# Kernel optimization log

Hardware: AMD Instinct MI355X
Metric: run time of the kernel (lower is better)

## Reference

```python
import jax, jax.numpy as jnp
import numpy as np

B, T, C, H = 2, 2048, 1024, 16

def setup_inputs() -> dict:
    key = jax.random.key(0)
    ks = jax.random.split(key, 6)
    s = 1.0 / np.sqrt(C)
    return {
        "x": jax.random.normal(ks[0], (B, T, C), jnp.float32),
        "Wq": jax.random.normal(ks[1], (C, C), jnp.float32) * s,
        "Wk": jax.random.normal(ks[2], (C, C), jnp.float32) * s,
        "Wv": jax.random.normal(ks[3], (C, C), jnp.float32) * s,
        "Wp": jax.random.normal(ks[4], (C, C), jnp.float32) * s,
        "bp": jnp.zeros((C,), jnp.float32),
    }

def reference(x, Wq, Wk, Wv, Wp, bp):
    b, t, c = x.shape
    hd = c // H  # head dim
    # Linear layers: torch nn.Linear computes x @ W.T
    def split_heads(y):
        return y.reshape(b, t, H, hd).transpose(0, 2, 1, 3)  # [B,H,T,hd]
    q = split_heads(x @ Wq.T)
    k = split_heads(x @ Wk.T)
    v = split_heads(x @ Wv.T)
    scale = hd ** -0.5
    wei = jnp.einsum('bhqd,bhkd->bhqk', q, k) * scale  # [B,H,T,T]
    causal = jnp.tril(jnp.ones((t, t), bool))
    wei = jnp.where(causal, wei, -jnp.inf)
    wei = jax.nn.softmax(wei, axis=-1)
    out = jnp.einsum('bhqk,bhkd->bhqd', wei, v)  # [B,H,T,hd]
    out = out.transpose(0, 2, 1, 3).reshape(b, t, c)
    return out @ Wp.T + bp
```

## Files before the change

### kernel.cpp

```cpp
#include <hip/hip_runtime.h>
#include <hip/hip_bf16.h>
#include <stdint.h>

#define B_ 2
#define T_ 2048
#define C_ 1024
#define H_ 16
#define HD_ 64
#define NTOK (B_*T_)

typedef __bf16 bf16;
typedef bf16 bf16x4 __attribute__((ext_vector_type(4)));
typedef bf16 bf16x8 __attribute__((ext_vector_type(8)));
typedef float f32x4 __attribute__((ext_vector_type(4)));

static __device__ __forceinline__ f32x4 mfma16(bf16x8 a, bf16x8 b, f32x4 c) {
  return __builtin_amdgcn_mfma_f32_16x16x32_bf16(a, b, c, 0, 0, 0);
}

static __device__ __forceinline__ void gload_lds16(const void* g, void* l) {
  __builtin_amdgcn_global_load_lds(
      (__attribute__((address_space(1))) void*)g,
      (__attribute__((address_space(3))) void*)l, 16, 0, 0);
}

static __device__ __forceinline__ uint32_t cvt_pk_bf16(float lo, float hi) {
  uint32_t r;
  asm("v_cvt_pk_bf16_f32 %0, %1, %2" : "=v"(r) : "v"(lo), "v"(hi));
  return r;
}

__global__ void cvt_all(const float* __restrict__ x,
                        const float* __restrict__ w0, const float* __restrict__ w1,
                        const float* __restrict__ w2, const float* __restrict__ w3,
                        bf16* __restrict__ xb,
                        bf16* __restrict__ d0, bf16* __restrict__ d1,
                        bf16* __restrict__ d2, bf16* __restrict__ d3) {
  const int i = blockIdx.x * 256 + threadIdx.x;
  const int y = blockIdx.y;
  const float* src;
  bf16* dst;
  size_t off4 = 0;
  if (y < 4) {
    src = x; dst = xb; off4 = (size_t)y << 18;
  } else if (y == 4) { src = w0; dst = d0; }
  else if (y == 5)   { src = w1; dst = d1; }
  else if (y == 6)   { src = w2; dst = d2; }
  else               { src = w3; dst = d3; }
  float4 v = reinterpret_cast<const float4*>(src)[off4 + i];
  bf16x4 o;
  o.x = (bf16)v.x; o.y = (bf16)v.y; o.z = (bf16)v.z; o.w = (bf16)v.w;
  reinterpret_cast<bf16x4*>(dst)[off4 + i] = o;
}

__global__ __launch_bounds__(256) void qkv_gemm(
    const bf16* __restrict__ X,
    const bf16* __restrict__ Wq, const bf16* __restrict__ Wk, const bf16* __restrict__ Wv,
    bf16* __restrict__ Q, bf16* __restrict__ K, bf16* __restrict__ VT) {
  __shared__ bf16 As[128 * 64];
  __shared__ bf16 Bs[128 * 64];
  const int z = blockIdx.z;
  const bf16* W = (z == 0) ? Wq : (z == 1) ? Wk : Wv;
  const int n0 = blockIdx.x * 128;
  const int o0 = blockIdx.y * 128;
  const int tid = threadIdx.x;
  const int lane = tid & 63;
  const int w = tid >> 6;
  const int wr = w >> 1, wc = w & 1;
  const int l15 = lane & 15, lhi = lane >> 4;
  const int x7 = l15 & 7;

  f32x4 acc[4][4] = {};

  for (int k0 = 0; k0 < C_; k0 += 64) {
    __syncthreads();
#pragma unroll
    for (int j = 0; j < 4; j++) {
      const int c = tid + j * 256;
      const int row = c >> 3;
      const int scol = ((c & 7) ^ (row & 7)) * 8;
      gload_lds16(X + (size_t)(n0 + row) * C_ + k0 + scol, (char*)As + c * 16);
      gload_lds16(W + (size_t)(o0 + row) * C_ + k0 + scol, (char*)Bs + c * 16);
    }
    __syncthreads();
    bf16x8 a[4][2], b[4][2];
#pragma unroll
    for (int m = 0; m < 4; m++) {
      const int row = wr * 64 + m * 16 + l15;
#pragma unroll
      for (int kk = 0; kk < 2; kk++)
        a[m][kk] = *reinterpret_cast<const bf16x8*>(
            (const char*)As + row * 128 + (((kk * 4 + lhi) ^ x7) * 16));
    }
#pragma unroll
    for (int n = 0; n < 4; n++) {
      const int row = wc * 64 + n * 16 + l15;
#pragma unroll
      for (int kk = 0; kk < 2; kk++)
        b[n][kk] = *reinterpret_cast<const bf16x8*>(
            (const char*)Bs + row * 128 + (((kk * 4 + lhi) ^ x7) * 16));
    }
#pragma unroll
    for (int m = 0; m < 4; m++)
#pragma unroll
      for (int n = 0; n < 4; n++)
#pragma unroll
        for (int kk = 0; kk < 2; kk++)
          acc[m][n] = mfma16(a[m][kk], b[n][kk], acc[m][n]);
  }

  const float QSCALE = 0.125f * 1.44269504f;
#pragma unroll
  for (int m = 0; m < 4; m++) {
#pragma unroll
    for (int n = 0; n < 4; n++) {
#pragma unroll
      for (int r = 0; r < 4; r++) {
        int tok = n0 + wr * 64 + m * 16 + lhi * 4 + r;
        int o = o0 + wc * 64 + n * 16 + l15;
        int bb = tok >> 11, t = tok & (T_ - 1);
        int h = o >> 6, d = o & 63;
        float v = acc[m][n][r];
        if (z == 0) {
          Q[((size_t)(bb * H_ + h) * T_ + t) * HD_ + d] = (bf16)(v * QSCALE);
        } else if (z == 1) {
          K[((size_t)(bb * H_ + h) * T_ + t) * HD_ + d] = (bf16)v;
        } else {
          VT[((size_t)(bb * H_ + h) * HD_ + d) * T_ + t] = (bf16)v;
        }
      }
    }
  }
}

__global__ __launch_bounds__(512) void attn_kernel(
    const bf16* __restrict__ Q, const bf16* __restrict__ K,
    const bf16* __restrict__ VT, bf16* __restrict__ att) {
  __shared__ bf16 KtL[2][64 * 64], VtL[2][64 * 64];
  __shared__ bf16 KtH[2][64 * 64], VtH[2][64 * 64];
  __shared__ bf16 P[8][32][72];
  __shared__ float Red[4][64][35];
  const int tid = threadIdx.x;
  const int lane = tid & 63;
  const int wid = tid >> 6;
  const int w = wid & 3;
  const int hig = wid >> 2;
  const int l15 = lane & 15, lhi = lane >> 4;
  const int bh = blockIdx.x;
  const int b = bh >> 4, h = bh & 15;
  const int by = (int)blockIdx.y;
  const int qt = (by < 8) ? (15 - by) : (by - 8);
  const int qw0 = qt * 128 + w * 32;
  const bf16* Qb = Q + (size_t)bh * T_ * HD_;
  const bf16* Kb = K + (size_t)bh * T_ * HD_;
  const bf16* Vb = VT + (size_t)bh * HD_ * T_;

  bf16 (*Kt)[64 * 64] = hig ? KtH : KtL;
  bf16 (*Vt)[64 * 64] = hig ? VtH : VtL;

  bf16x8 q[2][2];
#pragma unroll
  for (int m = 0; m < 2; m++)
#pragma unroll
    for (int kk = 0; kk < 2; kk++)
      q[m][kk] = *reinterpret_cast<const bf16x8*>(
          &Qb[(size_t)(qw0 + m * 16 + l15) * HD_ + kk * 32 + lhi * 8]);

  f32x4 o_acc[2][4] = {};
  float lsum[2] = {0.f, 0.f};

  const int nIter = qt + 1;
  const int tBeg = hig ? (qt + 1) : 0;
  const int ntw = ((qw0 + 31) >> 6) + 1;
  const int tEnd = hig ? ntw : (qt + 1);

  const int t256 = tid & 255;
  const int c0 = t256, c1 = t256 + 256;
  const int r0 = c0 >> 3, x0 = (c0 & 7) ^ (r0 & 7);
  const int r1 = c1 >> 3, x1 = (c1 & 7) ^ (r1 & 7);

#define STAGE(tt, bb)                                                                \
  do {                                                                               \
    int kv = (tt) * 64;                                                              \
    gload_lds16(Kb + (size_t)(kv + r0) * HD_ + x0 * 8, (char*)&Kt[bb][0] + c0 * 16); \
    gload_lds16(Kb + (size_t)(kv + r1) * HD_ + x1 * 8, (char*)&Kt[bb][0] + c1 * 16); \
    gload_lds16(Vb + (size_t)r0 * T_ + kv + x0 * 8, (char*)&Vt[bb][0] + c0 * 16);    \
    gload_lds16(Vb + (size_t)r1 * T_ + kv + x1 * 8, (char*)&Vt[bb][0] + c1 * 16);    \
  } while (0)

  STAGE(tBeg, 0);
  __syncthreads();

  for (int i = 0; i < nIter; ++i) {
    const int cur = i & 1;
    if (i + 1 < nIter) STAGE(tBeg + i + 1, cur ^ 1);
    const int tile = tBeg + i;
    if (tile < tEnd) {
      const int kv0 = tile * 64;
      f32x4 s[2][4] = {};
#pragma unroll
      for (int n = 0; n < 4; n++) {
        const int krow = n * 16 + l15;
#pragma unroll
        for (int kk = 0; kk < 2; kk++) {
          const int kx = (kk * 4 + lhi) ^ (l15 & 7);
          bf16x8 kf = *reinterpret_cast<const bf16x8*>(
              (const char*)&Kt[cur][0] + krow * 128 + kx * 16);
          s[0][n] = mfma16(kf, q[0][kk], s[0][n]);
          s[1][n] = mfma16(kf, q[1][kk], s[1][n]);
        }
      }

      if (kv0 + 63 > qw0) {
#pragma unroll
        for (int m = 0; m < 2; m++) {
          const int qrow = qw0 + m * 16 + l15;
#pragma unroll
          for (int n = 0; n < 4; n++) {
            const int key = kv0 + n * 16 + lhi * 4;
#pragma unroll
            for (int r = 0; r < 4; r++) {
              if (key + r > qrow) s[m][n][r] = -1e30f;
            }
          }
        }
      }
#pragma unroll
      for (int m = 0; m < 2; m++) {
        char* pw = (char*)&P[wid][m * 16 + l15][0];
#pragma unroll
        for (int n = 0; n < 4; n++) {
          float p0 = __builtin_amdgcn_exp2f(s[m][n][0]);
          float p1 = __builtin_amdgcn_exp2f(s[m][n][1]);
          float p2 = __builtin_amdgcn_exp2f(s[m][n][2]);
          float p3 = __builtin_amdgcn_exp2f(s[m][n][3]);
          lsum[m] += (p0 + p1) + (p2 + p3);
          uint32_t lo = cvt_pk_bf16(p0, p1);
          uint32_t hi = cvt_pk_bf16(p2, p3);
          *reinterpret_cast<uint2*>(pw + (4 * n + lhi) * 8) = make_uint2(lo, hi);
        }
      }
      bf16x8 pa[2][2];
#pragma unroll
      for (int m = 0; m < 2; m++)
#pragma unroll
        for (int kk = 0; kk < 2; kk++)
          pa[m][kk] = *reinterpret_cast<const bf16x8*>(
              (const char*)&P[wid][m * 16 + l15][0] + kk * 64 + lhi * 16);
#pragma unroll
      for (int n = 0; n < 4; n++) {
        const int vrow = n * 16 + l15;
#pragma unroll
        for (int kk = 0; kk < 2; kk++) {
          const int vx = (kk * 4 + lhi) ^ (l15 & 7);
          bf16x8 vf = *reinterpret_cast<const bf16x8*>(
              (const char*)&Vt[cur][0] + vrow * 128 + vx * 16);
          o_acc[0][n] = mfma16(pa[0][kk], vf, o_acc[0][n]);
          o_acc[1][n] = mfma16(pa[1][kk], vf, o_acc[1][n]);
        }
      }
    }
    __syncthreads();
  }
#undef STAGE

  if (hig) {
    float* rd = &Red[w][lane][0];
#pragma unroll
    for (int m = 0; m < 2; m++)
#pragma unroll
      for (int n = 0; n < 4; n++)
#pragma unroll
        for (int r = 0; r < 4; r++)
          rd[(m * 4 + n) * 4 + r] = o_acc[m][n][r];
    rd[32] = lsum[0];
    rd[33] = lsum[1];
  }
  __syncthreads();
  if (!hig) {
    const float* rd = &Red[w][lane][0];
#pragma unroll
    for (int m = 0; m < 2; m++) {
#pragma unroll
      for (int n = 0; n < 4; n++)
#pragma unroll
        for (int r = 0; r < 4; r++)
          o_acc[m][n][r] += rd[(m * 4 + n) * 4 + r];
      lsum[m] += rd[32 + m];
    }
    float lred[2];
#pragma unroll
    for (int m = 0; m < 2; m++) {
      float v = lsum[m];
      v += __shfl_xor(v, 16);
      v += __shfl_xor(v, 32);
      lred[m] = v;
    }
#pragma unroll
    for (int m = 0; m < 2; m++) {
#pragma unroll
      for (int r = 0; r < 4; r++) {
        float rs = __shfl(lred[m], (lane & 48) + lhi * 4 + r);
        float li = 1.f / rs;
        int t = qw0 + m * 16 + lhi * 4 + r;
#pragma unroll
        for (int n = 0; n < 4; n++) {
          int d = n * 16 + l15;
          att[((size_t)(b * T_ + t) * H_ + h) * HD_ + d] = (bf16)(o_acc[m][n][r] * li);
        }
      }
    }
  }
}

__global__ __launch_bounds__(256) void proj_gemm(
    const bf16* __restrict__ A, const bf16* __restrict__ Wp,
    const float* __restrict__ bp, float* __restrict__ out) {
  __shared__ bf16 As[128 * 64];
  __shared__ bf16 Bs[128 * 64];
  const int n0 = blockIdx.x * 128;
  const int o0 = blockIdx.y * 128;
  const int tid = threadIdx.x;
  const int lane = tid & 63;
  const int w = tid >> 6;
  const int wr = w >> 1, wc = w & 1;
  const int l15 = lane & 15, lhi = lane >> 4;
  const int x7 = l15 & 7;

  f32x4 acc[4][4] = {};

  for (int k0 = 0; k0 < C_; k0 += 64) {
    __syncthreads();
#pragma unroll
    for (int j = 0; j < 4; j++) {
      const int c = tid + j * 256;
      const int row = c >> 3;
      const int scol = ((c & 7) ^ (row & 7)) * 8;
      gload_lds16(A + (size_t)(n0 + row) * C_ + k0 + scol, (char*)As + c * 16);
      gload_lds16(Wp + (size_t)(o0 + row) * C_ + k0 + scol, (char*)Bs + c * 16);
    }
    __syncthreads();
    bf16x8 a[4][2], b[4][2];
#pragma unroll
    for (int m = 0; m < 4; m++) {
      const int row = wr * 64 + m * 16 + l15;
#pragma unroll
      for (int kk = 0; kk < 2; kk++)
        a[m][kk] = *reinterpret_cast<const bf16x8*>(
            (const char*)As + row * 128 + (((kk * 4 + lhi) ^ x7) * 16));
    }
#pragma unroll
    for (int n = 0; n < 4; n++) {
      const int row = wc * 64 + n * 16 + l15;
#pragma unroll
      for (int kk = 0; kk < 2; kk++)
        b[n][kk] = *reinterpret_cast<const bf16x8*>(
            (const char*)Bs + row * 128 + (((kk * 4 + lhi) ^ x7) * 16));
    }
#pragma unroll
    for (int m = 0; m < 4; m++)
#pragma unroll
      for (int n = 0; n < 4; n++)
#pragma unroll
        for (int kk = 0; kk < 2; kk++)
          acc[m][n] = mfma16(a[m][kk], b[n][kk], acc[m][n]);
  }

#pragma unroll
  for (int m = 0; m < 4; m++) {
#pragma unroll
    for (int n = 0; n < 4; n++) {
#pragma unroll
      for (int r = 0; r < 4; r++) {
        int tok = n0 + wr * 64 + m * 16 + lhi * 4 + r;
        int o = o0 + wc * 64 + n * 16 + l15;
        out[(size_t)tok * C_ + o] = acc[m][n][r] + bp[o];
      }
    }
  }
}

extern "C" void kernel_launch(void* const* d_in, const int* in_sizes, int n_in,
                              void* d_out, int out_size, void* d_ws, size_t ws_size,
                              hipStream_t stream) {
  const float* x  = (const float*)d_in[0];
  const float* Wq = (const float*)d_in[1];
  const float* Wk = (const float*)d_in[2];
  const float* Wv = (const float*)d_in[3];
  const float* Wp = (const float*)d_in[4];
  const float* bp = (const float*)d_in[5];
  float* out = (float*)d_out;

  char* ws = (char*)d_ws;
  size_t off = 0;
  bf16* xb  = (bf16*)(ws + off); off += (size_t)NTOK * C_ * 2;
  bf16* wqb = (bf16*)(ws + off); off += (size_t)C_ * C_ * 2;
  bf16* wkb = (bf16*)(ws + off); off += (size_t)C_ * C_ * 2;
  bf16* wvb = (bf16*)(ws + off); off += (size_t)C_ * C_ * 2;
  bf16* wpb = (bf16*)(ws + off); off += (size_t)C_ * C_ * 2;
  bf16* Qd  = (bf16*)(ws + off); off += (size_t)NTOK * C_ * 2;
  bf16* Kd  = (bf16*)(ws + off); off += (size_t)NTOK * C_ * 2;
  bf16* VTd = (bf16*)(ws + off); off += (size_t)NTOK * C_ * 2;
  bf16* att = (bf16*)(ws + off); off += (size_t)NTOK * C_ * 2;
  (void)ws_size; (void)out_size; (void)in_sizes; (void)n_in;

  cvt_all<<<dim3(1024, 8), 256, 0, stream>>>(x, Wq, Wk, Wv, Wp, xb, wqb, wkb, wvb, wpb);

  qkv_gemm<<<dim3(NTOK / 128, C_ / 128, 3), 256, 0, stream>>>(xb, wqb, wkb, wvb, Qd, Kd, VTd);
  attn_kernel<<<dim3(B_ * H_, 16), 512, 0, stream>>>(Qd, Kd, VTd, att);
  proj_gemm<<<dim3(NTOK / 128, C_ / 128), 256, 0, stream>>>(att, wpb, bp, out);
}
```

Baseline: 107.5 us.

## Triple-buffer LDS K-tiles in QKV and projection GEMMs with async prefetch

Restructures the QKV and output-projection GEMM main loops into a 3-stage software pipeline. Each stage holds a K=32 slice, and direct-to-LDS loads are issued two tiles ahead. Explicit vmcnt waits and a single barrier per iteration replace the old load-then-sync-then-compute pattern with two barriers per step. The aim is to overlap global memory latency with MFMA work. The cost is half as much compute per barrier, a new XOR swizzle for the 64-byte rows, and reliance on hand-written waitcnt ordering.

```diff
diff --git a/kernel.cpp b/kernel.cpp
--- a/kernel.cpp
+++ b/kernel.cpp
@@ -57,8 +57,8 @@
     const bf16* __restrict__ X,
     const bf16* __restrict__ Wq, const bf16* __restrict__ Wk, const bf16* __restrict__ Wv,
     bf16* __restrict__ Q, bf16* __restrict__ K, bf16* __restrict__ VT) {
-  __shared__ bf16 As[128 * 64];
-  __shared__ bf16 Bs[128 * 64];
+  __shared__ bf16 As[3][128 * 32];
+  __shared__ bf16 Bs[3][128 * 32];
   const int z = blockIdx.z;
   const bf16* W = (z == 0) ? Wq : (z == 1) ? Wk : Wv;
   const int n0 = blockIdx.x * 128;
@@ -68,46 +68,65 @@
   const int w = tid >> 6;
   const int wr = w >> 1, wc = w & 1;
   const int l15 = lane & 15, lhi = lane >> 4;
-  const int x7 = l15 & 7;
+  const int rsw = (l15 >> 1) & 3;
 
   f32x4 acc[4][4] = {};
 
-  for (int k0 = 0; k0 < C_; k0 += 64) {
-    __syncthreads();
-#pragma unroll
-    for (int j = 0; j < 4; j++) {
-      const int c = tid + j * 256;
-      const int row = c >> 3;
-      const int scol = ((c & 7) ^ (row & 7)) * 8;
-      gload_lds16(X + (size_t)(n0 + row) * C_ + k0 + scol, (char*)As + c * 16);
-      gload_lds16(W + (size_t)(o0 + row) * C_ + k0 + scol, (char*)Bs + c * 16);
-    }
-    __syncthreads();
-    bf16x8 a[4][2], b[4][2];
+  const int c0 = tid, c1 = tid + 256;
+  const int r0 = c0 >> 2, s0 = (c0 & 3) ^ ((r0 >> 1) & 3);
+  const int r1 = c1 >> 2, s1 = (c1 & 3) ^ ((r1 >> 1) & 3);
+
+#define STAGEQ(kt, bb)                                                               \
+  do {                                                                               \
+    gload_lds16(X + (size_t)(n0 + r0) * C_ + (kt) * 32 + s0 * 8, (char*)&As[bb][0] + c0 * 16); \
+    gload_lds16(X + (size_t)(n0 + r1) * C_ + (kt) * 32 + s1 * 8, (char*)&As[bb][0] + c1 * 16); \
+    gload_lds16(W + (size_t)(o0 + r0) * C_ + (kt) * 32 + s0 * 8, (char*)&Bs[bb][0] + c0 * 16); \
+    gload_lds16(W + (size_t)(o0 + r1) * C_ + (kt) * 32 + s1 * 8, (char*)&Bs[bb][0] + c1 * 16); \
+  } while (0)
+
+  STAGEQ(0, 0);
+  STAGEQ(1, 1);
+  asm volatile("s_waitcnt vmcnt(4)");
+  __builtin_amdgcn_sched_barrier(0);
+  __builtin_amdgcn_s_barrier();
+  __builtin_amdgcn_sched_barrier(0);
+
+  int cur = 0;
+  for (int T = 0; T < 32; ++T) {
+    int nb = cur + 2; if (nb >= 3) nb -= 3;
+    const bool pre = (T + 2 < 32);
+    if (pre) STAGEQ(T + 2, nb);
+
+    bf16x8 a[4], b[4];
 #pragma unroll
     for (int m = 0; m < 4; m++) {
       const int row = wr * 64 + m * 16 + l15;
-#pragma unroll
-      for (int kk = 0; kk < 2; kk++)
-        a[m][kk] = *reinterpret_cast<const bf16x8*>(
-            (const char*)As + row * 128 + (((kk * 4 + lhi) ^ x7) * 16));
+      a[m] = *reinterpret_cast<const bf16x8*>(
+          (const char*)&As[cur][0] + row * 64 + ((lhi ^ rsw) * 16));
     }
 #pragma unroll
     for (int n = 0; n < 4; n++) {
       const int row = wc * 64 + n * 16 + l15;
-#pragma unroll
-      for (int kk = 0; kk < 2; kk++)
-        b[n][kk] = *reinterpret_cast<const bf16x8*>(
-            (const char*)Bs + row * 128 + (((kk * 4 + lhi) ^ x7) * 16));
+      b[n] = *reinterpret_cast<const bf16x8*>(
+          (const char*)&Bs[cur][0] + row * 64 + ((lhi ^ rsw) * 16));
     }
 #pragma unroll
     for (int m = 0; m < 4; m++)
 #pragma unroll
       for (int n = 0; n < 4; n++)
-#pragma unroll
-        for (int kk = 0; kk < 2; kk++)
-          acc[m][n] = mfma16(a[m][kk], b[n][kk], acc[m][n]);
-  }
+        acc[m][n] = mfma16(a[m], b[n], acc[m][n]);
+
+    if (pre) {
+      asm volatile("s_waitcnt vmcnt(4)");
+    } else {
+      asm volatile("s_waitcnt vmcnt(0)");
+    }
+    __builtin_amdgcn_sched_barrier(0);
+    __builtin_amdgcn_s_barrier();
+    __builtin_amdgcn_sched_barrier(0);
+    cur = (cur == 2) ? 0 : cur + 1;
+  }
+#undef STAGEQ
 
   const float QSCALE = 0.125f * 1.44269504f;
 #pragma unroll
@@ -316,8 +335,8 @@
 __global__ __launch_bounds__(256) void proj_gemm(
     const bf16* __restrict__ A, const bf16* __restrict__ Wp,
     const float* __restrict__ bp, float* __restrict__ out) {
-  __shared__ bf16 As[128 * 64];
-  __shared__ bf16 Bs[128 * 64];
+  __shared__ bf16 As[3][128 * 32];
+  __shared__ bf16 Bs[3][128 * 32];
   const int n0 = blockIdx.x * 128;
   const int o0 = blockIdx.y * 128;
   const int tid = threadIdx.x;
@@ -325,46 +344,65 @@
   const int w = tid >> 6;
   const int wr = w >> 1, wc = w & 1;
   const int l15 = lane & 15, lhi = lane >> 4;
-  const int x7 = l15 & 7;
+  const int rsw = (l15 >> 1) & 3;
 
   f32x4 acc[4][4] = {};
 
-  for (int k0 = 0; k0 < C_; k0 += 64) {
-    __syncthreads();
-#pragma unroll
-    for (int j = 0; j < 4; j++) {
-      const int c = tid + j * 256;
-      const int row = c >> 3;
-      const int scol = ((c & 7) ^ (row & 7)) * 8;
-      gload_lds16(A + (size_t)(n0 + row) * C_ + k0 + scol, (char*)As + c * 16);
-      gload_lds16(Wp + (size_t)(o0 + row) * C_ + k0 + scol, (char*)Bs + c * 16);
-    }
-    __syncthreads();
-    bf16x8 a[4][2], b[4][2];
+  const int c0 = tid, c1 = tid + 256;
+  const int r0 = c0 >> 2, s0 = (c0 & 3) ^ ((r0 >> 1) & 3);
+  const int r1 = c1 >> 2, s1 = (c1 & 3) ^ ((r1 >> 1) & 3);
+
+#define STAGEP(kt, bb)                                                               \
+  do {                                                                               \
+    gload_lds16(A + (size_t)(n0 + r0) * C_ + (kt) * 32 + s0 * 8, (char*)&As[bb][0] + c0 * 16); \
+    gload_lds16(A + (size_t)(n0 + r1) * C_ + (kt) * 32 + s1 * 8, (char*)&As[bb][0] + c1 * 16); \
+    gload_lds16(Wp + (size_t)(o0 + r0) * C_ + (kt) * 32 + s0 * 8, (char*)&Bs[bb][0] + c0 * 16); \
+    gload_lds16(Wp + (size_t)(o0 + r1) * C_ + (kt) * 32 + s1 * 8, (char*)&Bs[bb][0] + c1 * 16); \
+  } while (0)
+
+  STAGEP(0, 0);
+  STAGEP(1, 1);
+  asm volatile("s_waitcnt vmcnt(4)");
+  __builtin_amdgcn_sched_barrier(0);
+  __builtin_amdgcn_s_barrier();
+  __builtin_amdgcn_sched_barrier(0);
+
+  int cur = 0;
+  for (int T = 0; T < 32; ++T) {
+    int nb = cur + 2; if (nb >= 3) nb -= 3;
+    const bool pre = (T + 2 < 32);
+    if (pre) STAGEP(T + 2, nb);
+
+    bf16x8 a[4], b[4];
 #pragma unroll
     for (int m = 0; m < 4; m++) {
       const int row = wr * 64 + m * 16 + l15;
-#pragma unroll
-      for (int kk = 0; kk < 2; kk++)
-        a[m][kk] = *reinterpret_cast<const bf16x8*>(
-            (const char*)As + row * 128 + (((kk * 4 + lhi) ^ x7) * 16));
+      a[m] = *reinterpret_cast<const bf16x8*>(
+          (const char*)&As[cur][0] + row * 64 + ((lhi ^ rsw) * 16));
     }
 #pragma unroll
     for (int n = 0; n < 4; n++) {
       const int row = wc * 64 + n * 16 + l15;
-#pragma unroll
-      for (int kk = 0; kk < 2; kk++)
-        b[n][kk] = *reinterpret_cast<const bf16x8*>(
-            (const char*)Bs + row * 128 + (((kk * 4 + lhi) ^ x7) * 16));
+      b[n] = *reinterpret_cast<const bf16x8*>(
+          (const char*)&Bs[cur][0] + row * 64 + ((lhi ^ rsw) * 16));
     }
 #pragma unroll
     for (int m = 0; m < 4; m++)
 #pragma unroll
       for (int n = 0; n < 4; n++)
-#pragma unroll
-        for (int kk = 0; kk < 2; kk++)
-          acc[m][n] = mfma16(a[m][kk], b[n][kk], acc[m][n]);
-  }
+        acc[m][n] = mfma16(a[m], b[n], acc[m][n]);
+
+    if (pre) {
+      asm volatile("s_waitcnt vmcnt(4)");
+    } else {
+      asm volatile("s_waitcnt vmcnt(0)");
+    }
+    __builtin_amdgcn_sched_barrier(0);
+    __builtin_amdgcn_s_barrier();
+    __builtin_amdgcn_sched_barrier(0);
+    cur = (cur == 2) ? 0 : cur + 1;
+  }
+#undef STAGEP
 
 #pragma unroll
   for (int m = 0; m < 4; m++) {
```

New measurement: 110.8 us. 3.1% more time.

## Shrink attention LDS footprint to fit multiple blocks per CU

Applied to the files above, without the earlier changes.

Replaces double-buffered K/V staging with single-buffered tiles, halves the P scratch by reusing one 16-row slice per m, and reuses the staging memory for the cross-wave output reduction with a lane-contiguous layout. The aim is to cut shared memory use so more workgroups can reside per CU and to reduce bank conflicts in the reduction. In exchange, the prefetch overlap of the next KV tile with compute is lost, and each iteration adds an extra barrier.

```diff
diff --git a/kernel.cpp b/kernel.cpp
--- a/kernel.cpp
+++ b/kernel.cpp
@@ -136,10 +136,9 @@
 __global__ __launch_bounds__(512) void attn_kernel(
     const bf16* __restrict__ Q, const bf16* __restrict__ K,
     const bf16* __restrict__ VT, bf16* __restrict__ att) {
-  __shared__ bf16 KtL[2][64 * 64], VtL[2][64 * 64];
-  __shared__ bf16 KtH[2][64 * 64], VtH[2][64 * 64];
-  __shared__ bf16 P[8][32][72];
-  __shared__ float Red[4][64][35];
+  __shared__ bf16 Stage[4][64 * 64];
+  __shared__ bf16 P[8][16][72];
+  __shared__ float RedL[4][2][64];
   const int tid = threadIdx.x;
   const int lane = tid & 63;
   const int wid = tid >> 6;
@@ -155,8 +154,8 @@
   const bf16* Kb = K + (size_t)bh * T_ * HD_;
   const bf16* Vb = VT + (size_t)bh * HD_ * T_;
 
-  bf16 (*Kt)[64 * 64] = hig ? KtH : KtL;
-  bf16 (*Vt)[64 * 64] = hig ? VtH : VtL;
+  bf16* Kt = &Stage[hig * 2 + 0][0];
+  bf16* Vt = &Stage[hig * 2 + 1][0];
 
   bf16x8 q[2][2];
 #pragma unroll
@@ -179,21 +178,19 @@
   const int r0 = c0 >> 3, x0 = (c0 & 7) ^ (r0 & 7);
   const int r1 = c1 >> 3, x1 = (c1 & 7) ^ (r1 & 7);
 
-#define STAGE(tt, bb)                                                                \
-  do {                                                                               \
-    int kv = (tt) * 64;                                                              \
-    gload_lds16(Kb + (size_t)(kv + r0) * HD_ + x0 * 8, (char*)&Kt[bb][0] + c0 * 16); \
-    gload_lds16(Kb + (size_t)(kv + r1) * HD_ + x1 * 8, (char*)&Kt[bb][0] + c1 * 16); \
-    gload_lds16(Vb + (size_t)r0 * T_ + kv + x0 * 8, (char*)&Vt[bb][0] + c0 * 16);    \
-    gload_lds16(Vb + (size_t)r1 * T_ + kv + x1 * 8, (char*)&Vt[bb][0] + c1 * 16);    \
+#define STAGE(tt)                                                                \
+  do {                                                                           \
+    int kv = (tt) * 64;                                                          \
+    gload_lds16(Kb + (size_t)(kv + r0) * HD_ + x0 * 8, (char*)Kt + c0 * 16);     \
+    gload_lds16(Kb + (size_t)(kv + r1) * HD_ + x1 * 8, (char*)Kt + c1 * 16);     \
+    gload_lds16(Vb + (size_t)r0 * T_ + kv + x0 * 8, (char*)Vt + c0 * 16);        \
+    gload_lds16(Vb + (size_t)r1 * T_ + kv + x1 * 8, (char*)Vt + c1 * 16);        \
   } while (0)
 
-  STAGE(tBeg, 0);
-  __syncthreads();
-
   for (int i = 0; i < nIter; ++i) {
-    const int cur = i & 1;
-    if (i + 1 < nIter) STAGE(tBeg + i + 1, cur ^ 1);
+    __syncthreads();
+    STAGE(tBeg + i);
+    __syncthreads();
     const int tile = tBeg + i;
     if (tile < tEnd) {
       const int kv0 = tile * 64;
@@ -205,7 +202,7 @@
         for (int kk = 0; kk < 2; kk++) {
           const int kx = (kk * 4 + lhi) ^ (l15 & 7);
           bf16x8 kf = *reinterpret_cast<const bf16x8*>(
-              (const char*)&Kt[cur][0] + krow * 128 + kx * 16);
+              (const char*)Kt + krow * 128 + kx * 16);
           s[0][n] = mfma16(kf, q[0][kk], s[0][n]);
           s[1][n] = mfma16(kf, q[1][kk], s[1][n]);
         }
@@ -225,9 +222,10 @@
           }
         }
       }
+      bf16x8 pa[2][2];
 #pragma unroll
       for (int m = 0; m < 2; m++) {
-        char* pw = (char*)&P[wid][m * 16 + l15][0];
+        char* pw = (char*)&P[wid][l15][0];
 #pragma unroll
         for (int n = 0; n < 4; n++) {
           float p0 = __builtin_amdgcn_exp2f(s[m][n][0]);
@@ -239,14 +237,11 @@
           uint32_t hi = cvt_pk_bf16(p2, p3);
           *reinterpret_cast<uint2*>(pw + (4 * n + lhi) * 8) = make_uint2(lo, hi);
         }
-      }
-      bf16x8 pa[2][2];
-#pragma unroll
-      for (int m = 0; m < 2; m++)
 #pragma unroll
         for (int kk = 0; kk < 2; kk++)
           pa[m][kk] = *reinterpret_cast<const bf16x8*>(
-              (const char*)&P[wid][m * 16 + l15][0] + kk * 64 + lhi * 16);
+              (const char*)&P[wid][l15][0] + kk * 64 + lhi * 16);
+      }
 #pragma unroll
       for (int n = 0; n < 4; n++) {
         const int vrow = n * 16 + l15;
@@ -254,39 +249,42 @@
         for (int kk = 0; kk < 2; kk++) {
           const int vx = (kk * 4 + lhi) ^ (l15 & 7);
           bf16x8 vf = *reinterpret_cast<const bf16x8*>(
-              (const char*)&Vt[cur][0] + vrow * 128 + vx * 16);
+              (const char*)Vt + vrow * 128 + vx * 16);
           o_acc[0][n] = mfma16(pa[0][kk], vf, o_acc[0][n]);
           o_acc[1][n] = mfma16(pa[1][kk], vf, o_acc[1][n]);
         }
       }
     }
-    __syncthreads();
   }
 #undef STAGE
 
+  __syncthreads();
+  float* Red2 = reinterpret_cast<float*>(&Stage[0][0]);
   if (hig) {
-    float* rd = &Red[w][lane][0];
 #pragma unroll
     for (int m = 0; m < 2; m++)
 #pragma unroll
       for (int n = 0; n < 4; n++)
 #pragma unroll
-        for (int r = 0; r < 4; r++)
-          rd[(m * 4 + n) * 4 + r] = o_acc[m][n][r];
-    rd[32] = lsum[0];
-    rd[33] = lsum[1];
+        for (int r = 0; r < 4; r++) {
+          const int v = (m * 4 + n) * 4 + r;
+          Red2[((size_t)w * 32 + v) * 64 + lane] = o_acc[m][n][r];
+        }
+    RedL[w][0][lane] = lsum[0];
+    RedL[w][1][lane] = lsum[1];
   }
   __syncthreads();
   if (!hig) {
-    const float* rd = &Red[w][lane][0];
 #pragma unroll
     for (int m = 0; m < 2; m++) {
 #pragma unroll
       for (int n = 0; n < 4; n++)
 #pragma unroll
-        for (int r = 0; r < 4; r++)
-          o_acc[m][n][r] += rd[(m * 4 + n) * 4 + r];
-      lsum[m] += rd[32 + m];
+        for (int r = 0; r < 4; r++) {
+          const int v = (m * 4 + n) * 4 + r;
+          o_acc[m][n][r] += Red2[((size_t)w * 32 + v) * 64 + lane];
+        }
+      lsum[m] += RedL[w][m][lane];
     }
     float lred[2];
 #pragma unroll
```

New measurement: 109.1 us. No clear change (+1.5%).
